# Kernel tuning notes

Measured on AMD Instinct MI355X. Metric: run time of the kernel, lower is better.

The kernel has to match this reference:

```python
import jax, jax.numpy as jnp
import numpy as np
import math

D_K = 64
DROP_P = 0.5

def setup_inputs() -> dict:
    key = jax.random.key(0)
    kq, kk, kv, km = jax.random.split(key, 4)
    B, S, d = 32, 2048, D_K
    Q = jax.random.normal(kq, (B, S, d), dtype=jnp.float32)
    K = jax.random.normal(kk, (B, S, d), dtype=jnp.float32)
    V = jax.random.normal(kv, (B, S, d), dtype=jnp.float32)
    # Bernoulli(keep_prob) mask for training-mode dropout (p=0.5)
    dropout_mask = jax.random.bernoulli(km, 1.0 - DROP_P, (B, S, S))
    return {"Q": Q, "K": K, "V": V, "dropout_mask": dropout_mask}

def reference(Q, K, V, dropout_mask):
    # attn = softmax(Q K^T / sqrt(d_k)); dropout; y = attn V
    scale = 1.0 / math.sqrt(D_K)
    scores = jnp.einsum('bqd,bkd->bqk', Q, K) * scale   # [B,S,S]
    attn = jax.nn.softmax(scores, axis=-1)
    keep_scale = 1.0 / (1.0 - DROP_P)
    attn = jnp.where(dropout_mask, attn * keep_scale, 0.0)
    y = jnp.einsum('bqk,bkd->bqd', attn, V)             # [B,S,d]
    return (y, attn)
```

## Files before the change

### kernel.cpp

```cpp
#include <hip/hip_runtime.h>
#include <hip/hip_bf16.h>
#include <stdint.h>

#define SQ 2048
#define DK 64
#define NB 32
#define TQ 16
#define EW 2064
#define SCL 0.18033688011112042f

typedef __attribute__((ext_vector_type(8))) short short8;
typedef __attribute__((ext_vector_type(4))) float f32x4;
typedef __attribute__((ext_vector_type(4))) unsigned u32x4;
typedef __attribute__((ext_vector_type(2))) unsigned u32x2;

__device__ __forceinline__ unsigned f2bf_u(float x) {
    unsigned u = __builtin_bit_cast(unsigned, x);
    u += 0x7fffu + ((u >> 16) & 1u);
    return u >> 16;
}
__device__ __forceinline__ float bf2f(unsigned h) {
    return __builtin_bit_cast(float, h << 16);
}
__device__ __forceinline__ float bf2f_hi(unsigned u) {
    return __builtin_bit_cast(float, u & 0xffff0000u);
}
__device__ __forceinline__ unsigned cvtpk_bf16(float lo, float hi) {
    unsigned r;
    asm("v_cvt_pk_bf16_f32 %0, %1, %2" : "=v"(r) : "v"(lo), "v"(hi));
    return r;
}
__device__ __forceinline__ void split8(const float* p, short8& h, short8& l) {
    f32x4 a = *(const f32x4*)p;
    f32x4 b = *(const f32x4*)(p + 4);
    #pragma unroll
    for (int j = 0; j < 4; ++j) {
        unsigned ua = f2bf_u(a[j]);
        h[j] = (short)ua; l[j] = (short)f2bf_u(a[j] - bf2f(ua));
        unsigned ub = f2bf_u(b[j]);
        h[j + 4] = (short)ub; l[j + 4] = (short)f2bf_u(b[j] - bf2f(ub));
    }
}

__global__ __launch_bounds__(256) void prep_kernel(
    const float* __restrict__ K, const float* __restrict__ V,
    unsigned short* __restrict__ Khi, unsigned short* __restrict__ Klo,
    unsigned short* __restrict__ Vt)
{
    __shared__ float vtile[64][65];
    const int t  = threadIdx.x;
    const int b  = blockIdx.x >> 5;
    const int s0 = (blockIdx.x & 31) << 6;
    const size_t base = ((size_t)b * SQ + s0) * DK + (size_t)t * 16;

    {
        short8 h0, l0, h1, l1;
        split8(K + base,     h0, l0);
        split8(K + base + 8, h1, l1);
        *(short8*)(Khi + base)     = h0;
        *(short8*)(Khi + base + 8) = h1;
        *(short8*)(Klo + base)     = l0;
        *(short8*)(Klo + base + 8) = l1;
    }
    {
        const int sr = t >> 2, dc = (t & 3) << 4;
        #pragma unroll
        for (int u = 0; u < 16; u += 4) {
            f32x4 v = *(const f32x4*)(V + base + u);
            vtile[sr][dc + u + 0] = v[0];
            vtile[sr][dc + u + 1] = v[1];
            vtile[sr][dc + u + 2] = v[2];
            vtile[sr][dc + u + 3] = v[3];
        }
    }
    __syncthreads();
    #pragma unroll
    for (int rep = 0; rep < 16; ++rep) {
        const int idx = rep * 256 + t;
        const int d = idx >> 6, s = idx & 63;
        Vt[((size_t)b * DK + d) * SQ + s0 + s] = (unsigned short)f2bf_u(vtile[s][d]);
    }
}

__global__ __launch_bounds__(256) void mkpack_kernel(
    const unsigned* __restrict__ Mk, unsigned* __restrict__ Mkb)
{
    const size_t w = (size_t)blockIdx.x * 256 + threadIdx.x;
    const unsigned* p = Mk + w * 32;
    unsigned bits = 0;
    #pragma unroll
    for (int j = 0; j < 8; ++j) {
        const u32x4 v = *(const u32x4*)(p + j * 4);
        bits |= (v[0] ? 1u : 0u) << (j * 4 + 0);
        bits |= (v[1] ? 1u : 0u) << (j * 4 + 1);
        bits |= (v[2] ? 1u : 0u) << (j * 4 + 2);
        bits |= (v[3] ? 1u : 0u) << (j * 4 + 3);
    }
    Mkb[w] = bits;
}

__global__ __launch_bounds__(512, 4) void sdpa_main(
    const float* __restrict__ Q, const unsigned short* __restrict__ Khi,
    const unsigned short* __restrict__ Klo, const unsigned short* __restrict__ Vt,
    const unsigned* __restrict__ Mkb, float* __restrict__ Yout, float* __restrict__ Aout)
{
    __shared__ __align__(16) unsigned short e_lds[TQ][EW];
    __shared__ float yp[4][TQ][16];
    __shared__ float rsum[8][TQ];
    __shared__ float i2s[TQ];

    const int tid  = threadIdx.x;
    const int lane = tid & 63;
    const int wv   = tid >> 6;
    const int m16  = lane & 15;
    const int kq   = lane >> 4;
    const int koff = kq * 8;

    const int bx  = blockIdx.x;
    const int xcd = bx & 7;
    const int j   = bx >> 3;
    const int b   = xcd * 4 + (j >> 7);
    const int q0  = (j & 127) * TQ;

    short8 qh[2], ql[2];
    {
        const float* qrow = Q + ((size_t)b * SQ + q0 + m16) * DK;
        split8(qrow + koff,      qh[0], ql[0]);
        split8(qrow + 32 + koff, qh[1], ql[1]);
    }

    const unsigned* mrow = Mkb + ((size_t)b * SQ + q0 + m16) * (SQ / 32) + wv * 8;
    const u32x4 mA = *(const u32x4*)mrow;
    const u32x4 mB = *(const u32x4*)(mrow + 4);

    float rs = 0.f;
    {
        const size_t krow = ((size_t)b * SQ + wv * 256 + m16) * DK;
        const unsigned short* khp = Khi + krow;
        const unsigned short* klp = Klo + krow;
        const int xw = (m16 & 7) << 3;
        #pragma unroll
        for (int t = 0; t < 16; ++t) {
            const int off = t * 16 * DK;
            const short8 kh0 = *(const short8*)(khp + off + koff);
            const short8 kh1 = *(const short8*)(khp + off + 32 + koff);
            const short8 kl0 = *(const short8*)(klp + off + koff);
            const short8 kl1 = *(const short8*)(klp + off + 32 + koff);
            f32x4 a0 = {0.f, 0.f, 0.f, 0.f};
            f32x4 a1 = {0.f, 0.f, 0.f, 0.f};
            a0 = __builtin_amdgcn_mfma_f32_16x16x32_bf16(kh0, qh[0], a0, 0, 0, 0);
            a1 = __builtin_amdgcn_mfma_f32_16x16x32_bf16(kh1, qh[1], a1, 0, 0, 0);
            a0 = __builtin_amdgcn_mfma_f32_16x16x32_bf16(kh0, ql[0], a0, 0, 0, 0);
            a1 = __builtin_amdgcn_mfma_f32_16x16x32_bf16(kh1, ql[1], a1, 0, 0, 0);
            a0 = __builtin_amdgcn_mfma_f32_16x16x32_bf16(kl0, qh[0], a0, 0, 0, 0);
            a1 = __builtin_amdgcn_mfma_f32_16x16x32_bf16(kl1, qh[1], a1, 0, 0, 0);
            const float e0 = __builtin_amdgcn_exp2f((a0[0] + a1[0]) * SCL);
            const float e1 = __builtin_amdgcn_exp2f((a0[1] + a1[1]) * SCL);
            const float e2 = __builtin_amdgcn_exp2f((a0[2] + a1[2]) * SCL);
            const float e3 = __builtin_amdgcn_exp2f((a0[3] + a1[3]) * SCL);
            rs += (e0 + e1) + (e2 + e3);
            const unsigned mword = (t < 8) ? mA[t >> 1] : mB[(t >> 1) - 4];
            const unsigned bits = mword >> ((t & 1) * 16 + kq * 4);
            const float p0 = (bits & 1u) ? e0 : 0.f;
            const float p1 = (bits & 2u) ? e1 : 0.f;
            const float p2 = (bits & 4u) ? e2 : 0.f;
            const float p3 = (bits & 8u) ? e3 : 0.f;
            u32x2 pk;
            pk[0] = cvtpk_bf16(p0, p1);
            pk[1] = cvtpk_bf16(p2, p3);
            *(u32x2*)&e_lds[m16][(wv * 256 + t * 16 + kq * 4) ^ xw] = pk;
        }
    }
    rs += __shfl_xor(rs, 16);
    rs += __shfl_xor(rs, 32);
    if (lane < 16) rsum[wv][lane] = rs;
    __syncthreads();
    if (tid < 16) {
        float s = 0.f;
        #pragma unroll
        for (int w = 0; w < 8; ++w) s += rsum[w][tid];
        i2s[tid] = 2.0f / s;
    }
    __syncthreads();

    const int cr = tid >> 5;
    const int cc = (tid & 31) * 8;
    const int xc = (cr & 7) << 3;
    const float i2 = i2s[cr];
    const size_t crow = ((size_t)b * SQ + q0 + cr) * SQ + cc;

    const int g    = wv >> 1;
    const int par  = wv & 1;
    const int xm   = (m16 & 7) << 3;
    const unsigned short* vrow = Vt + ((size_t)b * DK + g * 16 + m16) * SQ;
    f32x4 acc = {0.f, 0.f, 0.f, 0.f};

    #define CSTRIPE(s)                                                            \
    {                                                                             \
        const u32x4 ev = *(const u32x4*)&e_lds[cr][((s) * 256 + cc) ^ xc];        \
        f32x4 o0, o1;                                                             \
        o0[0] = bf2f(ev[0] & 0xffffu) * i2;  o0[1] = bf2f_hi(ev[0]) * i2;         \
        o0[2] = bf2f(ev[1] & 0xffffu) * i2;  o0[3] = bf2f_hi(ev[1]) * i2;         \
        o1[0] = bf2f(ev[2] & 0xffffu) * i2;  o1[1] = bf2f_hi(ev[2]) * i2;         \
        o1[2] = bf2f(ev[3] & 0xffffu) * i2;  o1[3] = bf2f_hi(ev[3]) * i2;         \
        *(f32x4*)(Aout + crow + (s) * 256)     = o0;                              \
        *(f32x4*)(Aout + crow + (s) * 256 + 4) = o1;                              \
    }
    #define PVCHUNK4(c0)                                                          \
    {                                                                             \
        _Pragma("unroll")                                                         \
        for (int c = (c0); c < (c0) + 4; ++c) {                                   \
            const int kl = par * 1024 + c * 32;                                   \
            const short8 af = *(const short8*)&e_lds[m16][(kl + koff) ^ xm];      \
            const short8 vf = *(const short8*)(vrow + kl + koff);                 \
            acc = __builtin_amdgcn_mfma_f32_16x16x32_bf16(af, vf, acc, 0, 0, 0);  \
        }                                                                         \
    }

    CSTRIPE(0) PVCHUNK4(0)
    CSTRIPE(1) PVCHUNK4(4)
    CSTRIPE(2) PVCHUNK4(8)
    CSTRIPE(3) PVCHUNK4(12)
    CSTRIPE(4) PVCHUNK4(16)
    CSTRIPE(5) PVCHUNK4(20)
    CSTRIPE(6) PVCHUNK4(24)
    CSTRIPE(7) PVCHUNK4(28)

    #undef PVCHUNK4
    #undef CSTRIPE

    if (par == 1) {
        #pragma unroll
        for (int r = 0; r < 4; ++r) yp[g][kq * 4 + r][m16] = acc[r];
    }
    __syncthreads();
    if (par == 0) {
        #pragma unroll
        for (int r = 0; r < 4; ++r) {
            const float yv = (acc[r] + yp[g][kq * 4 + r][m16]) * i2s[kq * 4 + r];
            Yout[((size_t)b * SQ + q0 + kq * 4 + r) * DK + g * 16 + m16] = yv;
        }
    }
}

extern "C" void kernel_launch(void* const* d_in, const int* in_sizes, int n_in,
                              void* d_out, int out_size, void* d_ws, size_t ws_size,
                              hipStream_t stream) {
    const float*    Q  = (const float*)d_in[0];
    const float*    K  = (const float*)d_in[1];
    const float*    V  = (const float*)d_in[2];
    const unsigned* Mk = (const unsigned*)d_in[3];
    float* Yout = (float*)d_out;
    float* Aout = (float*)d_out + (size_t)NB * SQ * DK;

    const size_t NEL = (size_t)NB * SQ * DK;
    unsigned short* Khi = (unsigned short*)d_ws;
    unsigned short* Klo = Khi + NEL;
    unsigned short* Vt  = Klo + NEL;
    unsigned*       Mkb = (unsigned*)(Vt + NEL);

    prep_kernel<<<dim3(NB * (SQ / 64)), dim3(256), 0, stream>>>(K, V, Khi, Klo, Vt);
    mkpack_kernel<<<dim3((NB * SQ * (SQ / 32)) / 256), dim3(256), 0, stream>>>(Mk, Mkb);
    sdpa_main<<<dim3(NB * (SQ / TQ)), dim3(512), 0, stream>>>(
        Q, Khi, Klo, Vt, Mkb, Yout, Aout);
}
```

Before: 561.7 us.

## Recompute scores in second pass to drop full-row LDS buffer, merge prep kernels

The main kernel no longer keeps the whole 16x2048 bf16 probability row in LDS. It runs QK^T twice: the first pass only accumulates row sums, and the second pass recomputes exp, applies the mask, writes attention straight to global memory with nontemporal stores, and feeds a small per-wave staging buffer into PV MFMAs. Each wave now covers all 64 output columns for its key slice, and the partial results are reduced across waves through LDS. The mask-packing kernel is merged into the prep kernel to save a launch. The cost is double the QK MFMA, exp and K-load work; in exchange LDS use shrinks, which can allow higher occupancy.

Measured after the change: 889.9 us. 1.58x slower.

```diff
diff --git a/kernel.cpp b/kernel.cpp
--- a/kernel.cpp
+++ b/kernel.cpp
@@ -6,7 +6,6 @@
 #define DK 64
 #define NB 32
 #define TQ 16
-#define EW 2064
 #define SCL 0.18033688011112042f
 
 typedef __attribute__((ext_vector_type(8))) short short8;
@@ -21,9 +20,6 @@
 }
 __device__ __forceinline__ float bf2f(unsigned h) {
     return __builtin_bit_cast(float, h << 16);
-}
-__device__ __forceinline__ float bf2f_hi(unsigned u) {
-    return __builtin_bit_cast(float, u & 0xffff0000u);
 }
 __device__ __forceinline__ unsigned cvtpk_bf16(float lo, float hi) {
     unsigned r;
@@ -44,11 +40,29 @@
 
 __global__ __launch_bounds__(256) void prep_kernel(
     const float* __restrict__ K, const float* __restrict__ V,
+    const unsigned* __restrict__ Mk,
     unsigned short* __restrict__ Khi, unsigned short* __restrict__ Klo,
-    unsigned short* __restrict__ Vt)
+    unsigned short* __restrict__ Vt, unsigned* __restrict__ Mkb)
 {
     __shared__ float vtile[64][65];
-    const int t  = threadIdx.x;
+    const int t = threadIdx.x;
+
+    if (blockIdx.x >= NB * 32) {
+        const size_t w = (size_t)(blockIdx.x - NB * 32) * 256 + t;
+        const unsigned* p = Mk + w * 32;
+        unsigned bits = 0;
+        #pragma unroll
+        for (int j = 0; j < 8; ++j) {
+            const u32x4 v = *(const u32x4*)(p + j * 4);
+            bits |= (v[0] ? 1u : 0u) << (j * 4 + 0);
+            bits |= (v[1] ? 1u : 0u) << (j * 4 + 1);
+            bits |= (v[2] ? 1u : 0u) << (j * 4 + 2);
+            bits |= (v[3] ? 1u : 0u) << (j * 4 + 3);
+        }
+        Mkb[w] = bits;
+        return;
+    }
+
     const int b  = blockIdx.x >> 5;
     const int s0 = (blockIdx.x & 31) << 6;
     const size_t base = ((size_t)b * SQ + s0) * DK + (size_t)t * 16;
@@ -82,30 +96,13 @@
     }
 }
 
-__global__ __launch_bounds__(256) void mkpack_kernel(
-    const unsigned* __restrict__ Mk, unsigned* __restrict__ Mkb)
-{
-    const size_t w = (size_t)blockIdx.x * 256 + threadIdx.x;
-    const unsigned* p = Mk + w * 32;
-    unsigned bits = 0;
-    #pragma unroll
-    for (int j = 0; j < 8; ++j) {
-        const u32x4 v = *(const u32x4*)(p + j * 4);
-        bits |= (v[0] ? 1u : 0u) << (j * 4 + 0);
-        bits |= (v[1] ? 1u : 0u) << (j * 4 + 1);
-        bits |= (v[2] ? 1u : 0u) << (j * 4 + 2);
-        bits |= (v[3] ? 1u : 0u) << (j * 4 + 3);
-    }
-    Mkb[w] = bits;
-}
-
 __global__ __launch_bounds__(512, 4) void sdpa_main(
     const float* __restrict__ Q, const unsigned short* __restrict__ Khi,
     const unsigned short* __restrict__ Klo, const unsigned short* __restrict__ Vt,
     const unsigned* __restrict__ Mkb, float* __restrict__ Yout, float* __restrict__ Aout)
 {
-    __shared__ __align__(16) unsigned short e_lds[TQ][EW];
-    __shared__ float yp[4][TQ][16];
+    __shared__ float yp[8][TQ][DK];
+    __shared__ __align__(16) unsigned short pstage[8][TQ][40];
     __shared__ float rsum[8][TQ];
     __shared__ float i2s[TQ];
 
@@ -129,18 +126,60 @@
         split8(qrow + 32 + koff, qh[1], ql[1]);
     }
 
+    const size_t krow = ((size_t)b * SQ + wv * 256 + m16) * DK;
+    const unsigned short* khp = Khi + krow;
+    const unsigned short* klp = Klo + krow;
+
+    float rs = 0.f;
+    #pragma unroll
+    for (int t = 0; t < 16; ++t) {
+        const int off = t * 16 * DK;
+        const short8 kh0 = *(const short8*)(khp + off + koff);
+        const short8 kh1 = *(const short8*)(khp + off + 32 + koff);
+        const short8 kl0 = *(const short8*)(klp + off + koff);
+        const short8 kl1 = *(const short8*)(klp + off + 32 + koff);
+        f32x4 a0 = {0.f, 0.f, 0.f, 0.f};
+        f32x4 a1 = {0.f, 0.f, 0.f, 0.f};
+        a0 = __builtin_amdgcn_mfma_f32_16x16x32_bf16(kh0, qh[0], a0, 0, 0, 0);
+        a1 = __builtin_amdgcn_mfma_f32_16x16x32_bf16(kh1, qh[1], a1, 0, 0, 0);
+        a0 = __builtin_amdgcn_mfma_f32_16x16x32_bf16(kh0, ql[0], a0, 0, 0, 0);
+        a1 = __builtin_amdgcn_mfma_f32_16x16x32_bf16(kh1, ql[1], a1, 0, 0, 0);
+        a0 = __builtin_amdgcn_mfma_f32_16x16x32_bf16(kl0, qh[0], a0, 0, 0, 0);
+        a1 = __builtin_amdgcn_mfma_f32_16x16x32_bf16(kl1, qh[1], a1, 0, 0, 0);
+        rs += (__builtin_amdgcn_exp2f((a0[0] + a1[0]) * SCL)
+             + __builtin_amdgcn_exp2f((a0[1] + a1[1]) * SCL))
+            + (__builtin_amdgcn_exp2f((a0[2] + a1[2]) * SCL)
+             + __builtin_amdgcn_exp2f((a0[3] + a1[3]) * SCL));
+    }
+    rs += __shfl_xor(rs, 16);
+    rs += __shfl_xor(rs, 32);
+    if (lane < 16) rsum[wv][lane] = rs;
+    __syncthreads();
+    if (tid < 16) {
+        float s = 0.f;
+        #pragma unroll
+        for (int w = 0; w < 8; ++w) s += rsum[w][tid];
+        i2s[tid] = 2.0f / s;
+    }
+    __syncthreads();
+
     const unsigned* mrow = Mkb + ((size_t)b * SQ + q0 + m16) * (SQ / 32) + wv * 8;
     const u32x4 mA = *(const u32x4*)mrow;
     const u32x4 mB = *(const u32x4*)(mrow + 4);
-
-    float rs = 0.f;
-    {
-        const size_t krow = ((size_t)b * SQ + wv * 256 + m16) * DK;
-        const unsigned short* khp = Khi + krow;
-        const unsigned short* klp = Klo + krow;
-        const int xw = (m16 & 7) << 3;
-        #pragma unroll
-        for (int t = 0; t < 16; ++t) {
+    const float i2r = i2s[m16];
+    float* arow = Aout + ((size_t)b * SQ + q0 + m16) * SQ + wv * 256 + kq * 4;
+    const unsigned short* vb0 = Vt + ((size_t)b * DK + m16) * SQ + wv * 256 + koff;
+
+    f32x4 ac0 = {0.f, 0.f, 0.f, 0.f};
+    f32x4 ac1 = {0.f, 0.f, 0.f, 0.f};
+    f32x4 ac2 = {0.f, 0.f, 0.f, 0.f};
+    f32x4 ac3 = {0.f, 0.f, 0.f, 0.f};
+
+    #pragma unroll
+    for (int pp = 0; pp < 8; ++pp) {
+        #pragma unroll
+        for (int s2 = 0; s2 < 2; ++s2) {
+            const int t = pp * 2 + s2;
             const int off = t * 16 * DK;
             const short8 kh0 = *(const short8*)(khp + off + koff);
             const short8 kh1 = *(const short8*)(khp + off + 32 + koff);
@@ -158,88 +197,49 @@
             const float e1 = __builtin_amdgcn_exp2f((a0[1] + a1[1]) * SCL);
             const float e2 = __builtin_amdgcn_exp2f((a0[2] + a1[2]) * SCL);
             const float e3 = __builtin_amdgcn_exp2f((a0[3] + a1[3]) * SCL);
-            rs += (e0 + e1) + (e2 + e3);
             const unsigned mword = (t < 8) ? mA[t >> 1] : mB[(t >> 1) - 4];
             const unsigned bits = mword >> ((t & 1) * 16 + kq * 4);
             const float p0 = (bits & 1u) ? e0 : 0.f;
             const float p1 = (bits & 2u) ? e1 : 0.f;
             const float p2 = (bits & 4u) ? e2 : 0.f;
             const float p3 = (bits & 8u) ? e3 : 0.f;
+            f32x4 o = {p0 * i2r, p1 * i2r, p2 * i2r, p3 * i2r};
+            __builtin_nontemporal_store(o, (f32x4*)(arow + t * 16));
             u32x2 pk;
             pk[0] = cvtpk_bf16(p0, p1);
             pk[1] = cvtpk_bf16(p2, p3);
-            *(u32x2*)&e_lds[m16][(wv * 256 + t * 16 + kq * 4) ^ xw] = pk;
-        }
-    }
-    rs += __shfl_xor(rs, 16);
-    rs += __shfl_xor(rs, 32);
-    if (lane < 16) rsum[wv][lane] = rs;
-    __syncthreads();
-    if (tid < 16) {
-        float s = 0.f;
-        #pragma unroll
-        for (int w = 0; w < 8; ++w) s += rsum[w][tid];
-        i2s[tid] = 2.0f / s;
-    }
-    __syncthreads();
-
-    const int cr = tid >> 5;
-    const int cc = (tid & 31) * 8;
-    const int xc = (cr & 7) << 3;
-    const float i2 = i2s[cr];
-    const size_t crow = ((size_t)b * SQ + q0 + cr) * SQ + cc;
-
-    const int g    = wv >> 1;
-    const int par  = wv & 1;
-    const int xm   = (m16 & 7) << 3;
-    const unsigned short* vrow = Vt + ((size_t)b * DK + g * 16 + m16) * SQ;
-    f32x4 acc = {0.f, 0.f, 0.f, 0.f};
-
-    #define CSTRIPE(s)                                                            \
-    {                                                                             \
-        const u32x4 ev = *(const u32x4*)&e_lds[cr][((s) * 256 + cc) ^ xc];        \
-        f32x4 o0, o1;                                                             \
-        o0[0] = bf2f(ev[0] & 0xffffu) * i2;  o0[1] = bf2f_hi(ev[0]) * i2;         \
-        o0[2] = bf2f(ev[1] & 0xffffu) * i2;  o0[3] = bf2f_hi(ev[1]) * i2;         \
-        o1[0] = bf2f(ev[2] & 0xffffu) * i2;  o1[1] = bf2f_hi(ev[2]) * i2;         \
-        o1[2] = bf2f(ev[3] & 0xffffu) * i2;  o1[3] = bf2f_hi(ev[3]) * i2;         \
-        *(f32x4*)(Aout + crow + (s) * 256)     = o0;                              \
-        *(f32x4*)(Aout + crow + (s) * 256 + 4) = o1;                              \
-    }
-    #define PVCHUNK4(c0)                                                          \
-    {                                                                             \
-        _Pragma("unroll")                                                         \
-        for (int c = (c0); c < (c0) + 4; ++c) {                                   \
-            const int kl = par * 1024 + c * 32;                                   \
-            const short8 af = *(const short8*)&e_lds[m16][(kl + koff) ^ xm];      \
-            const short8 vf = *(const short8*)(vrow + kl + koff);                 \
-            acc = __builtin_amdgcn_mfma_f32_16x16x32_bf16(af, vf, acc, 0, 0, 0);  \
-        }                                                                         \
-    }
-
-    CSTRIPE(0) PVCHUNK4(0)
-    CSTRIPE(1) PVCHUNK4(4)
-    CSTRIPE(2) PVCHUNK4(8)
-    CSTRIPE(3) PVCHUNK4(12)
-    CSTRIPE(4) PVCHUNK4(16)
-    CSTRIPE(5) PVCHUNK4(20)
-    CSTRIPE(6) PVCHUNK4(24)
-    CSTRIPE(7) PVCHUNK4(28)
-
-    #undef PVCHUNK4
-    #undef CSTRIPE
-
-    if (par == 1) {
-        #pragma unroll
-        for (int r = 0; r < 4; ++r) yp[g][kq * 4 + r][m16] = acc[r];
-    }
-    __syncthreads();
-    if (par == 0) {
-        #pragma unroll
-        for (int r = 0; r < 4; ++r) {
-            const float yv = (acc[r] + yp[g][kq * 4 + r][m16]) * i2s[kq * 4 + r];
-            Yout[((size_t)b * SQ + q0 + kq * 4 + r) * DK + g * 16 + m16] = yv;
-        }
+            *(u32x2*)&pstage[wv][m16][s2 * 16 + kq * 4] = pk;
+        }
+        const short8 af = *(const short8*)&pstage[wv][m16][koff];
+        const unsigned short* vb = vb0 + pp * 32;
+        ac0 = __builtin_amdgcn_mfma_f32_16x16x32_bf16(af, *(const short8*)vb, ac0, 0, 0, 0);
+        ac1 = __builtin_amdgcn_mfma_f32_16x16x32_bf16(af, *(const short8*)(vb + 16 * SQ), ac1, 0, 0, 0);
+        ac2 = __builtin_amdgcn_mfma_f32_16x16x32_bf16(af, *(const short8*)(vb + 32 * SQ), ac2, 0, 0, 0);
+        ac3 = __builtin_amdgcn_mfma_f32_16x16x32_bf16(af, *(const short8*)(vb + 48 * SQ), ac3, 0, 0, 0);
+    }
+
+    #pragma unroll
+    for (int r = 0; r < 4; ++r) {
+        const int q = kq * 4 + r;
+        yp[wv][q][m16]      = ac0[r];
+        yp[wv][q][16 + m16] = ac1[r];
+        yp[wv][q][32 + m16] = ac2[r];
+        yp[wv][q][48 + m16] = ac3[r];
+    }
+    __syncthreads();
+
+    {
+        const int q = tid >> 5;
+        const int d = (tid & 31) * 2;
+        float s0 = 0.f, s1 = 0.f;
+        #pragma unroll
+        for (int w = 0; w < 8; ++w) {
+            s0 += yp[w][q][d];
+            s1 += yp[w][q][d + 1];
+        }
+        const float i2 = i2s[q];
+        float2 yv = {s0 * i2, s1 * i2};
+        *(float2*)(Yout + ((size_t)b * SQ + q0 + q) * DK + d) = yv;
     }
 }
 
@@ -259,8 +259,9 @@
     unsigned short* Vt  = Klo + NEL;
     unsigned*       Mkb = (unsigned*)(Vt + NEL);
 
-    prep_kernel<<<dim3(NB * (SQ / 64)), dim3(256), 0, stream>>>(K, V, Khi, Klo, Vt);
-    mkpack_kernel<<<dim3((NB * SQ * (SQ / 32)) / 256), dim3(256), 0, stream>>>(Mk, Mkb);
+    const int NPREP = NB * 32;
+    const int NMKP  = (int)((size_t)NB * SQ * (SQ / 32) / 256);
+    prep_kernel<<<dim3(NPREP + NMKP), dim3(256), 0, stream>>>(K, V, Mk, Khi, Klo, Vt, Mkb);
     sdpa_main<<<dim3(NB * (SQ / TQ)), dim3(512), 0, stream>>>(
         Q, Khi, Klo, Vt, Mkb, Yout, Aout);
 }
```
